# Performance work log

Measured on AMD Instinct MI355X. Metric: run time of the kernel, lower is better.

Reference implementation:

```python
import jax, jax.numpy as jnp
import numpy as np

EMBED_DIM = 1024
NUM_HEADS = 16
HEAD_DIM = EMBED_DIM // NUM_HEADS


def setup_inputs() -> dict:
    key = jax.random.key(0)
    ks = jax.random.split(key, 9)
    B, S, E = 2, 2048, EMBED_DIM
    scale = 1.0 / np.sqrt(E)
    inp = {
        "x": jax.random.normal(ks[0], (B, S, E), dtype=jnp.float32),
        "Wq": jax.random.normal(ks[1], (E, E), dtype=jnp.float32) * scale,
        "bq": jnp.zeros((E,), dtype=jnp.float32),
        "Wk": jax.random.normal(ks[2], (E, E), dtype=jnp.float32) * scale,
        "bk": jnp.zeros((E,), dtype=jnp.float32),
        "Wv": jax.random.normal(ks[3], (E, E), dtype=jnp.float32) * scale,
        "bv": jnp.zeros((E,), dtype=jnp.float32),
        "Wo": jax.random.normal(ks[4], (E, E), dtype=jnp.float32) * scale,
        "bo": jnp.zeros((E,), dtype=jnp.float32),
    }
    return inp


def reference(x, Wq, bq, Wk, bk, Wv, bv, Wo, bo):
    B, S, E = x.shape
    H, D = NUM_HEADS, HEAD_DIM
    sm_scale = D ** (-0.5)

    def proj(W, b):
        # torch Linear: x @ W.T + b ; reshape to [B, H, S, D]
        y = jnp.einsum("bse,fe->bsf", x, W) + b
        return y.reshape(B, S, H, D).transpose(0, 2, 1, 3)

    q = proj(Wq, bq)  # [B, H, S, D]
    k = proj(Wk, bk)
    v = proj(Wv, bv)

    scores = jnp.einsum("bhqd,bhkd->bhqk", q, k) * sm_scale  # [B, H, S, S]
    attn = jax.nn.softmax(scores, axis=-1)
    o = jnp.einsum("bhqk,bhkd->bhqd", attn, v)  # [B, H, S, D]
    o = o.transpose(0, 2, 1, 3).reshape(B, S, E)
    return jnp.einsum("bse,fe->bsf", o, Wo) + bo
```

## Files before the change

kernel.cpp:

```cpp
#include <hip/hip_runtime.h>
#include <hip/hip_fp16.h>
#include <stdint.h>


typedef _Float16 f16;
typedef _Float16 f16x8 __attribute__((ext_vector_type(8)));
typedef _Float16 f16x4v __attribute__((ext_vector_type(4)));
typedef float f32x4 __attribute__((ext_vector_type(4)));
typedef int i32x4 __attribute__((ext_vector_type(4)));

#define BQ  2
#define SEQ 2048
#define EMB 1024
#define NH  16
#define HD  64
#define MM  (BQ * SEQ)

__device__ __forceinline__ void gld_lds16(const void* g, void* l) {
  __builtin_amdgcn_global_load_lds(
      (const __attribute__((address_space(1))) void*)g,
      (__attribute__((address_space(3))) void*)l, 16, 0, 0);
}

__device__ __forceinline__ void stage128x64(const f16* __restrict__ src,
                                            int ld, f16* lds, int tid) {
#pragma unroll
  for (int it = 0; it < 4; ++it) {
    int idx = it * 256 + tid;
    int r = idx >> 3, c = idx & 7;
    int sc = c ^ (r & 7);
    gld_lds16(src + (size_t)r * ld + sc * 8, lds + idx * 8);
  }
}

__device__ __forceinline__ f16x8 pack8(float a0, float a1, float a2, float a3,
                                       float b0, float b1, float b2, float b3) {
  i32x4 w;
  w.x = __builtin_bit_cast(int, __builtin_amdgcn_cvt_pkrtz(a0, a1));
  w.y = __builtin_bit_cast(int, __builtin_amdgcn_cvt_pkrtz(a2, a3));
  w.z = __builtin_bit_cast(int, __builtin_amdgcn_cvt_pkrtz(b0, b1));
  w.w = __builtin_bit_cast(int, __builtin_amdgcn_cvt_pkrtz(b2, b3));
  return __builtin_bit_cast(f16x8, w);
}

__global__ void cvtAll(const float* __restrict__ x, const float* __restrict__ w0,
                       const float* __restrict__ w1, const float* __restrict__ w2,
                       const float* __restrict__ w3, f16* __restrict__ dst) {
  int i = blockIdx.x * blockDim.x + threadIdx.x;
  const float* s;
  int off;
  if (i < (1 << 19)) {
    s = x; off = i;
  } else {
    int j = i - (1 << 19);
    int w = j >> 17, o = j & ((1 << 17) - 1);
    s = (w == 0) ? w0 : (w == 1) ? w1 : (w == 2) ? w2 : w3;
    off = o;
  }
  float4 v0 = ((const float4*)s)[2 * off];
  float4 v1 = ((const float4*)s)[2 * off + 1];
  ((f16x8*)dst)[i] = pack8(v0.x, v0.y, v0.z, v0.w, v1.x, v1.y, v1.z, v1.w);
}

template <int MODE>
__global__ __launch_bounds__(256, 2) void gemm_bt(
    const f16* __restrict__ A, const f16* __restrict__ W0,
    const f16* __restrict__ W1, const f16* __restrict__ W2,
    const float* __restrict__ b0, const float* __restrict__ b1,
    const float* __restrict__ b2, f16* __restrict__ o0, f16* __restrict__ o1,
    f16* __restrict__ o2, float* __restrict__ fo) {
  __shared__ __align__(16) f16 As[128 * 64];
  __shared__ __align__(16) f16 Bs[128 * 64];

  const int tid = threadIdx.x, lane = tid & 63, wid = tid >> 6;
  const int o = blockIdx.x;
  const int cx = o & 7, j = o >> 3;
  const int bx = 4 * cx + (j & 3);
  int by, z;
  if (MODE == 0) { int yz = j >> 2; by = yz & 7; z = yz >> 3; }
  else           { by = j >> 2; z = 0; }
  const f16* W = (z == 0) ? W0 : (z == 1 ? W1 : W2);
  const float* bia = (z == 0) ? b0 : (z == 1 ? b1 : b2);
  f16* outp = (z == 0) ? o0 : (z == 1 ? o1 : o2);
  const int row0 = bx * 128, col0 = by * 128;
  const int wr = (wid >> 1) * 64, wc = (wid & 1) * 64;
  const int rb = lane & 15, gq = lane >> 4, sw = lane & 7;

  f32x4 acc[4][4] = {};

  for (int kt = 0; kt < EMB / 64; ++kt) {
    __syncthreads();
    stage128x64(A + (size_t)row0 * EMB + kt * 64, EMB, As, tid);
    stage128x64(W + (size_t)col0 * EMB + kt * 64, EMB, Bs, tid);
    asm volatile("s_waitcnt vmcnt(0)" ::: "memory");
    __syncthreads();
#pragma unroll
    for (int kk = 0; kk < 2; ++kk) {
      f16x8 av[4], bv[4];
#pragma unroll
      for (int f = 0; f < 4; ++f) {
        av[f] = *(const f16x8*)(As + (wr + f * 16 + rb) * 64 +
                                (((kk * 4 + gq) ^ sw) << 3));
        bv[f] = *(const f16x8*)(Bs + (wc + f * 16 + rb) * 64 +
                                (((kk * 4 + gq) ^ sw) << 3));
      }
#pragma unroll
      for (int fi = 0; fi < 4; ++fi)
#pragma unroll
        for (int fj = 0; fj < 4; ++fj)
          acc[fi][fj] = __builtin_amdgcn_mfma_f32_16x16x32_f16(
              av[fi], bv[fj], acc[fi][fj], 0, 0, 0);
    }
  }

  float bias[4];
#pragma unroll
  for (int fj = 0; fj < 4; ++fj) bias[fj] = bia[col0 + wc + fj * 16 + rb];
  const float scale = (MODE == 0 && z == 0) ? 0.18033688011112042f : 1.0f;
#pragma unroll
  for (int fi = 0; fi < 4; ++fi) {
#pragma unroll
    for (int i = 0; i < 4; ++i) {
      int row = row0 + wr + fi * 16 + gq * 4 + i;
#pragma unroll
      for (int fj = 0; fj < 4; ++fj) {
        int col = col0 + wc + fj * 16 + rb;
        float v = (acc[fi][fj][i] + bias[fj]) * scale;
        if (MODE == 0) {
          int bb = row >> 11, s = row & (SEQ - 1);
          int h = col >> 6, d = col & 63;
          outp[(((size_t)(bb * NH + h)) * SEQ + s) * HD + d] = (f16)v;
        } else {
          fo[(size_t)row * EMB + col] = v;
        }
      }
    }
  }
}

__global__ __launch_bounds__(256) void vtrans(const f16* __restrict__ V,
                                              f16* __restrict__ Vt) {
  __shared__ f16 T[64][72];
  const int tid = threadIdx.x;
  const int s0 = blockIdx.x * 64, bh = blockIdx.y;
  const f16* Vh = V + (size_t)bh * SEQ * HD;
  f16* Vth = Vt + (size_t)bh * HD * SEQ;
#pragma unroll
  for (int it = 0; it < 2; ++it) {
    int idx = it * 256 + tid;
    int r = idx >> 3, c0 = (idx & 7) * 8;
    *(f16x8*)&T[r][c0] = *(const f16x8*)(Vh + (size_t)(s0 + r) * HD + c0);
  }
  __syncthreads();
#pragma unroll
  for (int it = 0; it < 2; ++it) {
    int idx = it * 256 + tid;
    int d = idx >> 3, a = idx & 7;
    f16x8 v;
#pragma unroll
    for (int j = 0; j < 8; ++j) v[j] = T[a * 8 + j][d];
    const int base = ((a >> 2) << 5) + ((a & 1) << 4) + (((a >> 1) & 1) << 2);
    f16* dst = Vth + (size_t)d * SEQ + s0 + base;
    f16x4v w0, w1;
#pragma unroll
    for (int j = 0; j < 4; ++j) { w0[j] = v[j]; w1[j] = v[4 + j]; }
    *(f16x4v*)dst = w0;
    *(f16x4v*)(dst + 8) = w1;
  }
}

__global__ __launch_bounds__(256, 2) void attn_fwd(const f16* __restrict__ Q,
                                                   const f16* __restrict__ K,
                                                   const f16* __restrict__ Vt,
                                                   f16* __restrict__ O) {
  __shared__ __align__(16) f16 Ks[2][2][64 * 64];
  __shared__ __align__(16) f16 Vs[2][2][64 * 64];

  const int tid = threadIdx.x, lane = tid & 63;
  const int wid = tid >> 6;
  const int orig = blockIdx.x;
  const int swz = ((orig & 7) << 6) + (orig >> 3);
  const int qt = swz & 15, bh = swz >> 4;
  const f16* Qh = Q + (size_t)bh * SEQ * HD;
  const f16* Kh = K + (size_t)bh * SEQ * HD;
  const f16* Vth = Vt + (size_t)bh * HD * SEQ;
  const int q0 = qt * 128 + wid * 32;
  const int rb = lane & 15, gq = lane >> 4, sw = lane & 7;

  f16x8 aq[2][2];
#pragma unroll
  for (int qf = 0; qf < 2; ++qf)
#pragma unroll
    for (int kk = 0; kk < 2; ++kk)
      aq[qf][kk] = *(const f16x8*)(Qh + (size_t)(q0 + qf * 16 + rb) * HD +
                                   kk * 32 + gq * 8);
  asm volatile("s_waitcnt vmcnt(0)" ::: "memory");

  const int srow = tid >> 3, scol = (tid & 7) ^ (srow & 7);
  const f16* Kg0 = Kh + (size_t)srow * HD + scol * 8;
  const f16* Vg0 = Vth + (size_t)srow * SEQ + scol * 8;

  const int NT2 = SEQ / 128;
#pragma unroll
  for (int sub = 0; sub < 2; ++sub) {
    const f16* kg = Kg0 + (size_t)sub * 64 * HD;
    const f16* vg = Vg0 + sub * 64;
    gld_lds16(kg,            &Ks[0][sub][tid * 8]);
    gld_lds16(kg + 32 * HD,  &Ks[0][sub][(tid + 256) * 8]);
    gld_lds16(vg,            &Vs[0][sub][tid * 8]);
    gld_lds16(vg + 32 * SEQ, &Vs[0][sub][(tid + 256) * 8]);
  }

  f16x8 ones;
#pragma unroll
  for (int j = 0; j < 8; ++j) ones[j] = (f16)1.0f;

  f32x4 oaccA[2][4] = {};
  f32x4 oaccB[2][4] = {};
  f32x4 lacc[2] = {};

  for (int t = 0; t < NT2; ++t) {
    __builtin_amdgcn_s_barrier();
    __builtin_amdgcn_sched_barrier(0);
    {
      const int tp = (t + 1 < NT2) ? t + 1 : NT2 - 1;
      const int ns = (t + 1) & 1;
#pragma unroll
      for (int sub = 0; sub < 2; ++sub) {
        const f16* kg = Kg0 + (size_t)(2 * tp + sub) * 64 * HD;
        const f16* vg = Vg0 + (2 * tp + sub) * 64;
        gld_lds16(kg,            &Ks[ns][sub][tid * 8]);
        gld_lds16(kg + 32 * HD,  &Ks[ns][sub][(tid + 256) * 8]);
        gld_lds16(vg,            &Vs[ns][sub][tid * 8]);
        gld_lds16(vg + 32 * SEQ, &Vs[ns][sub][(tid + 256) * 8]);
      }
      asm volatile("s_waitcnt vmcnt(8)" ::: "memory");
    }
    __builtin_amdgcn_s_barrier();
    __builtin_amdgcn_sched_barrier(0);

    const int cs = t & 1;
    const f16* Kb0 = &Ks[cs][0][0];
    const f16* Kb1 = &Ks[cs][1][0];
    const f16* Vb0 = &Vs[cs][0][0];
    const f16* Vb1 = &Vs[cs][1][0];

    __builtin_amdgcn_s_setprio(1);

    f32x4 s0_[2][4] = {};
#pragma unroll
    for (int kk = 0; kk < 2; ++kk) {
      f16x8 bk[4];
#pragma unroll
      for (int cf = 0; cf < 4; ++cf)
        bk[cf] = *(const f16x8*)(Kb0 + (cf * 16 + rb) * 64 +
                                 (((kk * 4 + gq) ^ sw) << 3));
#pragma unroll
      for (int qf = 0; qf < 2; ++qf)
#pragma unroll
        for (int cf = 0; cf < 4; ++cf)
          s0_[qf][cf] = __builtin_amdgcn_mfma_f32_16x16x32_f16(
              bk[cf], aq[qf][kk], s0_[qf][cf], 0, 0, 0);
    }

    f16x8 bp0[2][2];
#pragma unroll
    for (int qf = 0; qf < 2; ++qf)
#pragma unroll
      for (int g = 0; g < 2; ++g) {
        float e0 = __builtin_amdgcn_exp2f(s0_[qf][2 * g][0]);
        float e1 = __builtin_amdgcn_exp2f(s0_[qf][2 * g][1]);
        float e2 = __builtin_amdgcn_exp2f(s0_[qf][2 * g][2]);
        float e3 = __builtin_amdgcn_exp2f(s0_[qf][2 * g][3]);
        float f0 = __builtin_amdgcn_exp2f(s0_[qf][2 * g + 1][0]);
        float f1 = __builtin_amdgcn_exp2f(s0_[qf][2 * g + 1][1]);
        float f2 = __builtin_amdgcn_exp2f(s0_[qf][2 * g + 1][2]);
        float f3 = __builtin_amdgcn_exp2f(s0_[qf][2 * g + 1][3]);
        bp0[qf][g] = pack8(e0, e1, e2, e3, f0, f1, f2, f3);
      }

    f32x4 s1_[2][4] = {};
#pragma unroll
    for (int kk = 0; kk < 2; ++kk) {
      f16x8 bk[4];
#pragma unroll
      for (int cf = 0; cf < 4; ++cf)
        bk[cf] = *(const f16x8*)(Kb1 + (cf * 16 + rb) * 64 +
                                 (((kk * 4 + gq) ^ sw) << 3));
#pragma unroll
      for (int qf = 0; qf < 2; ++qf)
#pragma unroll
        for (int cf = 0; cf < 4; ++cf)
          s1_[qf][cf] = __builtin_amdgcn_mfma_f32_16x16x32_f16(
              bk[cf], aq[qf][kk], s1_[qf][cf], 0, 0, 0);
    }

#pragma unroll
    for (int g = 0; g < 2; ++g) {
      lacc[0] = __builtin_amdgcn_mfma_f32_16x16x32_f16(bp0[0][g], ones,
                                                       lacc[0], 0, 0, 0);
      lacc[1] = __builtin_amdgcn_mfma_f32_16x16x32_f16(bp0[1][g], ones,
                                                       lacc[1], 0, 0, 0);
#pragma unroll
      for (int df = 0; df < 4; ++df) {
        f16x8 vb = *(const f16x8*)(Vb0 + (df * 16 + rb) * 64 +
                                   (((g * 4 + gq) ^ sw) << 3));
        oaccA[0][df] = __builtin_amdgcn_mfma_f32_16x16x32_f16(
            bp0[0][g], vb, oaccA[0][df], 0, 0, 0);
        oaccA[1][df] = __builtin_amdgcn_mfma_f32_16x16x32_f16(
            bp0[1][g], vb, oaccA[1][df], 0, 0, 0);
      }
    }

    f16x8 bp1[2][2];
#pragma unroll
    for (int qf = 0; qf < 2; ++qf)
#pragma unroll
      for (int g = 0; g < 2; ++g) {
        float e0 = __builtin_amdgcn_exp2f(s1_[qf][2 * g][0]);
        float e1 = __builtin_amdgcn_exp2f(s1_[qf][2 * g][1]);
        float e2 = __builtin_amdgcn_exp2f(s1_[qf][2 * g][2]);
        float e3 = __builtin_amdgcn_exp2f(s1_[qf][2 * g][3]);
        float f0 = __builtin_amdgcn_exp2f(s1_[qf][2 * g + 1][0]);
        float f1 = __builtin_amdgcn_exp2f(s1_[qf][2 * g + 1][1]);
        float f2 = __builtin_amdgcn_exp2f(s1_[qf][2 * g + 1][2]);
        float f3 = __builtin_amdgcn_exp2f(s1_[qf][2 * g + 1][3]);
        bp1[qf][g] = pack8(e0, e1, e2, e3, f0, f1, f2, f3);
      }

#pragma unroll
    for (int g = 0; g < 2; ++g) {
      lacc[0] = __builtin_amdgcn_mfma_f32_16x16x32_f16(bp1[0][g], ones,
                                                       lacc[0], 0, 0, 0);
      lacc[1] = __builtin_amdgcn_mfma_f32_16x16x32_f16(bp1[1][g], ones,
                                                       lacc[1], 0, 0, 0);
#pragma unroll
      for (int df = 0; df < 4; ++df) {
        f16x8 vb = *(const f16x8*)(Vb1 + (df * 16 + rb) * 64 +
                                   (((g * 4 + gq) ^ sw) << 3));
        oaccB[0][df] = __builtin_amdgcn_mfma_f32_16x16x32_f16(
            bp1[0][g], vb, oaccB[0][df], 0, 0, 0);
        oaccB[1][df] = __builtin_amdgcn_mfma_f32_16x16x32_f16(
            bp1[1][g], vb, oaccB[1][df], 0, 0, 0);
      }
    }

    __builtin_amdgcn_s_setprio(0);
  }
  asm volatile("s_waitcnt vmcnt(0)" ::: "memory");

  const int b = bh >> 4, h = bh & 15;
#pragma unroll
  for (int qf = 0; qf < 2; ++qf)
#pragma unroll
    for (int i = 0; i < 4; ++i) {
      const float inv = 1.0f / lacc[qf][i];
      const int s = q0 + qf * 16 + gq * 4 + i;
      f16* orow = O + ((size_t)(b * SEQ + s)) * EMB + h * 64 + rb;
#pragma unroll
      for (int df = 0; df < 4; ++df)
        orow[df * 16] =
            (f16)((oaccA[qf][df][i] + oaccB[qf][df][i]) * inv);
    }
}

extern "C" void kernel_launch(void* const* d_in, const int* in_sizes, int n_in,
                              void* d_out, int out_size, void* d_ws,
                              size_t ws_size, hipStream_t stream) {
  const float* x = (const float*)d_in[0];
  const float* Wq = (const float*)d_in[1];
  const float* bq = (const float*)d_in[2];
  const float* Wk = (const float*)d_in[3];
  const float* bk = (const float*)d_in[4];
  const float* Wv = (const float*)d_in[5];
  const float* bv = (const float*)d_in[6];
  const float* Wo = (const float*)d_in[7];
  const float* bo = (const float*)d_in[8];
  float* out = (float*)d_out;

  const size_t NX = (size_t)MM * EMB;
  const size_t NW = (size_t)EMB * EMB;

  f16* xh  = (f16*)d_ws;
  f16* wqh = xh + NX;
  f16* wkh = wqh + NW;
  f16* wvh = wkh + NW;
  f16* woh = wvh + NW;
  f16* Qw  = woh + NW;
  f16* Kw  = Qw + NX;
  f16* Vw  = Kw + NX;
  f16* Vtw = Vw + NX;
  f16* Ow  = Vtw + NX;

  cvtAll<<<dim3(4096), 256, 0, stream>>>(x, Wq, Wk, Wv, Wo, xh);

  gemm_bt<0><<<dim3(768), 256, 0, stream>>>(
      xh, wqh, wkh, wvh, bq, bk, bv, Qw, Kw, Vw, nullptr);

  vtrans<<<dim3(SEQ / 64, BQ * NH), 256, 0, stream>>>(Vw, Vtw);

  attn_fwd<<<dim3(512), 256, 0, stream>>>(Qw, Kw, Vtw, Ow);

  gemm_bt<1><<<dim3(256), 256, 0, stream>>>(
      Ow, woh, woh, woh, bo, bo, bo, nullptr, nullptr, nullptr, out);
}
```

Measured before the change: 103.2 us.

## Fuse V transpose into QKV GEMM by swapping operands for V tiles

For the V projection blocks, the GEMM swaps its A and B operands so that it computes V^T directly. The epilogue then writes V^T in the permuted sequence layout that attn_fwd expects, with the bias applied per row. This removes the separate vtrans kernel launch along with its extra read and write of V. The cost is that the V-tile stores now have a stride of SEQ per element across lanes, and the epilogue gets more complex with per-row bias loads.

```diff
diff --git a/kernel.cpp b/kernel.cpp
--- a/kernel.cpp
+++ b/kernel.cpp
@@ -83,6 +83,9 @@
   const float* bia = (z == 0) ? b0 : (z == 1 ? b1 : b2);
   f16* outp = (z == 0) ? o0 : (z == 1 ? o1 : o2);
   const int row0 = bx * 128, col0 = by * 128;
+  const bool vswap = (MODE == 0 && z == 2);
+  const f16* Asrc = vswap ? W + (size_t)col0 * EMB : A + (size_t)row0 * EMB;
+  const f16* Bsrc = vswap ? A + (size_t)row0 * EMB : W + (size_t)col0 * EMB;
   const int wr = (wid >> 1) * 64, wc = (wid & 1) * 64;
   const int rb = lane & 15, gq = lane >> 4, sw = lane & 7;
 
@@ -90,8 +93,8 @@
 
   for (int kt = 0; kt < EMB / 64; ++kt) {
     __syncthreads();
-    stage128x64(A + (size_t)row0 * EMB + kt * 64, EMB, As, tid);
-    stage128x64(W + (size_t)col0 * EMB + kt * 64, EMB, Bs, tid);
+    stage128x64(Asrc + kt * 64, EMB, As, tid);
+    stage128x64(Bsrc + kt * 64, EMB, Bs, tid);
     asm volatile("s_waitcnt vmcnt(0)" ::: "memory");
     __syncthreads();
 #pragma unroll
@@ -114,58 +117,43 @@
   }
 
   float bias[4];
-#pragma unroll
-  for (int fj = 0; fj < 4; ++fj) bias[fj] = bia[col0 + wc + fj * 16 + rb];
+  if (!vswap) {
+#pragma unroll
+    for (int fj = 0; fj < 4; ++fj) bias[fj] = bia[col0 + wc + fj * 16 + rb];
+  }
   const float scale = (MODE == 0 && z == 0) ? 0.18033688011112042f : 1.0f;
 #pragma unroll
   for (int fi = 0; fi < 4; ++fi) {
 #pragma unroll
     for (int i = 0; i < 4; ++i) {
-      int row = row0 + wr + fi * 16 + gq * 4 + i;
+      const int lr = wr + fi * 16 + gq * 4 + i;
+      const float brow = vswap ? bia[col0 + lr] : 0.f;
 #pragma unroll
       for (int fj = 0; fj < 4; ++fj) {
-        int col = col0 + wc + fj * 16 + rb;
-        float v = (acc[fi][fj][i] + bias[fj]) * scale;
+        const int lc = wc + fj * 16 + rb;
+        float v = acc[fi][fj][i] + (vswap ? brow : bias[fj]);
+        v *= scale;
         if (MODE == 0) {
-          int bb = row >> 11, s = row & (SEQ - 1);
-          int h = col >> 6, d = col & 63;
-          outp[(((size_t)(bb * NH + h)) * SEQ + s) * HD + d] = (f16)v;
+          if (vswap) {
+            int e = col0 + lr, sg = row0 + lc;
+            int h = e >> 6, d = e & 63;
+            int b = sg >> 11, sl = sg & (SEQ - 1);
+            int u = sl & 63;
+            int p = ((u >> 5) << 5) + (((u >> 2) & 3) << 3) +
+                    (((u >> 4) & 1) << 2) + (u & 3);
+            int spos = (sl & ~63) | p;
+            outp[((size_t)(b * NH + h) * HD + d) * SEQ + spos] = (f16)v;
+          } else {
+            int row = row0 + lr, col = col0 + lc;
+            int bb = row >> 11, s = row & (SEQ - 1);
+            int h = col >> 6, d = col & 63;
+            outp[(((size_t)(bb * NH + h)) * SEQ + s) * HD + d] = (f16)v;
+          }
         } else {
-          fo[(size_t)row * EMB + col] = v;
+          fo[(size_t)(row0 + lr) * EMB + col0 + lc] = v;
         }
       }
     }
-  }
-}
-
-__global__ __launch_bounds__(256) void vtrans(const f16* __restrict__ V,
-                                              f16* __restrict__ Vt) {
-  __shared__ f16 T[64][72];
-  const int tid = threadIdx.x;
-  const int s0 = blockIdx.x * 64, bh = blockIdx.y;
-  const f16* Vh = V + (size_t)bh * SEQ * HD;
-  f16* Vth = Vt + (size_t)bh * HD * SEQ;
-#pragma unroll
-  for (int it = 0; it < 2; ++it) {
-    int idx = it * 256 + tid;
-    int r = idx >> 3, c0 = (idx & 7) * 8;
-    *(f16x8*)&T[r][c0] = *(const f16x8*)(Vh + (size_t)(s0 + r) * HD + c0);
-  }
-  __syncthreads();
-#pragma unroll
-  for (int it = 0; it < 2; ++it) {
-    int idx = it * 256 + tid;
-    int d = idx >> 3, a = idx & 7;
-    f16x8 v;
-#pragma unroll
-    for (int j = 0; j < 8; ++j) v[j] = T[a * 8 + j][d];
-    const int base = ((a >> 2) << 5) + ((a & 1) << 4) + (((a >> 1) & 1) << 2);
-    f16* dst = Vth + (size_t)d * SEQ + s0 + base;
-    f16x4v w0, w1;
-#pragma unroll
-    for (int j = 0; j < 4; ++j) { w0[j] = v[j]; w1[j] = v[4 + j]; }
-    *(f16x4v*)dst = w0;
-    *(f16x4v*)(dst + 8) = w1;
   }
 }
 
@@ -388,16 +376,13 @@
   f16* woh = wvh + NW;
   f16* Qw  = woh + NW;
   f16* Kw  = Qw + NX;
-  f16* Vw  = Kw + NX;
-  f16* Vtw = Vw + NX;
+  f16* Vtw = Kw + NX;
   f16* Ow  = Vtw + NX;
 
   cvtAll<<<dim3(4096), 256, 0, stream>>>(x, Wq, Wk, Wv, Wo, xh);
 
   gemm_bt<0><<<dim3(768), 256, 0, stream>>>(
-      xh, wqh, wkh, wvh, bq, bk, bv, Qw, Kw, Vw, nullptr);
-
-  vtrans<<<dim3(SEQ / 64, BQ * NH), 256, 0, stream>>>(Vw, Vtw);
+      xh, wqh, wkh, wvh, bq, bk, bv, Qw, Kw, Vtw, nullptr);
 
   attn_fwd<<<dim3(512), 256, 0, stream>>>(Qw, Kw, Vtw, Ow);
 
```

Result: no change. 101.7 us, median of 3 (-1.5%).
